# Performance work log

Hardware: AMD Instinct MI355X
Metric: run time of the kernel (lower is better)

The kernel has to match this reference:

```python
import jax, jax.numpy as jnp
import numpy as np

B, S, D, H = 2, 2048, 1024, 16
HID = 1024  # hidden_dim

def setup_inputs() -> dict:
    key = jax.random.key(0)
    ks = jax.random.split(key, 9)
    sc = 1.0 / np.sqrt(D)
    return {
        "x": jax.random.normal(ks[0], (B, S, D), dtype=jnp.float32),
        "Wq": jax.random.normal(ks[1], (HID, D), dtype=jnp.float32) * sc,
        "bq": jnp.zeros((HID,), dtype=jnp.float32),
        "Wk": jax.random.normal(ks[2], (HID, D), dtype=jnp.float32) * sc,
        "bk": jnp.zeros((HID,), dtype=jnp.float32),
        "Wv": jax.random.normal(ks[3], (HID, D), dtype=jnp.float32) * sc,
        "bv": jnp.zeros((HID,), dtype=jnp.float32),
        "Wo": jax.random.normal(ks[4], (D, HID), dtype=jnp.float32) * (1.0 / np.sqrt(HID)),
        "bo": jnp.zeros((D,), dtype=jnp.float32),
    }

def reference(x, Wq, bq, Wk, bk, Wv, bv, Wo, bo):
    num_heads = H
    hd = HID // num_heads
    q = x @ Wq.T + bq  # [B,S,HID]
    k = x @ Wk.T + bk
    v = x @ Wv.T + bv
    # [B,S,H,hd] -> [B,H,S,hd]
    q = q.reshape(B, S, num_heads, hd).transpose(0, 2, 1, 3)
    k = k.reshape(B, S, num_heads, hd).transpose(0, 2, 1, 3)
    v = v.reshape(B, S, num_heads, hd).transpose(0, 2, 1, 3)
    # NOTE: original scales by sqrt(hidden_dim), not sqrt(head_dim)
    scores = jnp.einsum('bhqd,bhkd->bhqk', q, k) / jnp.sqrt(jnp.float32(HID))
    attn = jax.nn.softmax(scores, axis=-1)
    out = jnp.einsum('bhqk,bhkd->bhqd', attn, v)  # [B,H,S,hd]
    out = out.transpose(0, 2, 1, 3).reshape(B, S, HID)
    return out @ Wo.T + bo
```

## Files before the change

### kernel.cpp

```cpp
#include <hip/hip_runtime.h>
#include <hip/hip_bf16.h>


typedef __bf16 bf16;
typedef bf16 bf16x8 __attribute__((ext_vector_type(8)));
typedef float f32x4 __attribute__((ext_vector_type(4)));

#define MFMA16(Af, Bf, Cf) __builtin_amdgcn_mfma_f32_16x16x32_bf16((Af), (Bf), (Cf), 0, 0, 0)

__device__ __forceinline__ void gl_lds16(const void* g, void* l) {
    __builtin_amdgcn_global_load_lds(
        (const __attribute__((address_space(1))) void*)g,
        (__attribute__((address_space(3))) void*)l, 16, 0, 0);
}

__device__ __forceinline__ float exp2_fast(float x) {
    float r; asm("v_exp_f32 %0, %1" : "=v"(r) : "v"(x)); return r;
}

__global__ __launch_bounds__(256) void cvt_all(
    const float* __restrict__ x, const float* __restrict__ Wq,
    const float* __restrict__ Wk, const float* __restrict__ Wv,
    const float* __restrict__ Wo,
    bf16* __restrict__ xb, bf16* __restrict__ wqb, bf16* __restrict__ wkb,
    bf16* __restrict__ wvb, bf16* __restrict__ wob)
{
    const size_t i8 = ((size_t)blockIdx.x * 256 + threadIdx.x) * 8;
    const float* src; bf16* dst; size_t off;
    if (i8 < 4194304)      { src = x;  dst = xb;  off = i8; }
    else if (i8 < 5242880) { src = Wq; dst = wqb; off = i8 - 4194304; }
    else if (i8 < 6291456) { src = Wk; dst = wkb; off = i8 - 5242880; }
    else if (i8 < 7340032) { src = Wv; dst = wvb; off = i8 - 6291456; }
    else                   { src = Wo; dst = wob; off = i8 - 7340032; }
    f32x4 a = *reinterpret_cast<const f32x4*>(src + off);
    f32x4 b = *reinterpret_cast<const f32x4*>(src + off + 4);
    bf16x8 o;
    o[0]=(bf16)a[0]; o[1]=(bf16)a[1]; o[2]=(bf16)a[2]; o[3]=(bf16)a[3];
    o[4]=(bf16)b[0]; o[5]=(bf16)b[1]; o[6]=(bf16)b[2]; o[7]=(bf16)b[3];
    *reinterpret_cast<bf16x8*>(dst + off) = o;
}

__global__ __launch_bounds__(512) void qkv_gemm(
    const bf16* __restrict__ xb,
    const bf16* __restrict__ wqb, const bf16* __restrict__ wkb,
    const bf16* __restrict__ wvb,
    const float* __restrict__ bq, const float* __restrict__ bk,
    const float* __restrict__ bv,
    bf16* __restrict__ qo, bf16* __restrict__ ko, bf16* __restrict__ vo)
{
    __shared__ bf16 As[128 * 64];
    __shared__ bf16 Bs[128 * 64];

    const int which = blockIdx.y;
    const bf16* W     = (which == 0) ? wqb : (which == 1) ? wkb : wvb;
    const float* bia  = (which == 0) ? bq : (which == 1) ? bk : bv;
    bf16* outp        = (which == 0) ? qo : (which == 1) ? ko : vo;
    const float scale = (which == 0) ? 0.04508422f : 1.0f;

    const int bid0 = blockIdx.x;
    const int xcd = bid0 & 7, j = bid0 >> 3;
    const int tm = xcd * 4 + (j & 3);
    const int tn = j >> 2;
    const int m0 = tm * 128, n0 = tn * 128;

    const int t = threadIdx.x;
    const int l = t & 63, w = t >> 6;
    const int wr = w >> 1, wc = w & 1;
    const int lg = l >> 4, lr = l & 15;

    f32x4 acc[2][4];
#pragma unroll
    for (int i = 0; i < 2; ++i)
#pragma unroll
        for (int jj = 0; jj < 4; ++jj)
            acc[i][jj] = (f32x4){0.f, 0.f, 0.f, 0.f};

    char* AsB = (char*)As;
    char* BsB = (char*)Bs;

    for (int kt = 0; kt < 1024; kt += 64) {
#pragma unroll
        for (int i = 0; i < 2; ++i) {
            const int c = w * 128 + i * 64 + l;
            const int row = c >> 3, cc = (c & 7) ^ (row & 7);
            gl_lds16(xb + (size_t)(m0 + row) * 1024 + kt + cc * 8, AsB + (w * 128 + i * 64) * 16);
            gl_lds16(W  + (size_t)(n0 + row) * 1024 + kt + cc * 8, BsB + (w * 128 + i * 64) * 16);
        }
        __syncthreads();

#pragma unroll
        for (int ks = 0; ks < 2; ++ks) {
            bf16x8 af[2], bff[4];
#pragma unroll
            for (int i = 0; i < 2; ++i) {
                const int ar = wr * 32 + i * 16 + lr;
                af[i]  = *reinterpret_cast<bf16x8*>(AsB + ar * 128 + ((ks * 64 + (lg << 4)) ^ ((ar & 7) << 4)));
            }
#pragma unroll
            for (int i = 0; i < 4; ++i) {
                const int br = wc * 64 + i * 16 + lr;
                bff[i] = *reinterpret_cast<bf16x8*>(BsB + br * 128 + ((ks * 64 + (lg << 4)) ^ ((br & 7) << 4)));
            }
            if (which == 2) {
#pragma unroll
                for (int mi = 0; mi < 2; ++mi)
#pragma unroll
                    for (int ni = 0; ni < 4; ++ni)
                        acc[mi][ni] = MFMA16(bff[ni], af[mi], acc[mi][ni]);
            } else {
#pragma unroll
                for (int mi = 0; mi < 2; ++mi)
#pragma unroll
                    for (int ni = 0; ni < 4; ++ni)
                        acc[mi][ni] = MFMA16(af[mi], bff[ni], acc[mi][ni]);
            }
        }
        __syncthreads();
    }

    if (which == 2) {
#pragma unroll
        for (int ni = 0; ni < 4; ++ni) {
#pragma unroll
            for (int mi = 0; mi < 2; ++mi) {
#pragma unroll
                for (int r = 0; r < 4; ++r) {
                    const int col = n0 + wc * 64 + ni * 16 + lg * 4 + r;
                    const int h = col >> 6, d = col & 63;
                    const int rowg = m0 + wr * 32 + mi * 16 + lr;
                    const int b = rowg >> 11, s = rowg & 2047;
                    const int key = s & 127;
                    const int pos = (key & 96) | ((key & 12) << 1) | ((key & 16) >> 2) | (key & 3);
                    const float v = acc[mi][ni][r] + bia[col];
                    outp[((size_t)(b * 16 + h) * 64 + d) * 2048 + (s & ~127) + pos] = (bf16)v;
                }
            }
        }
    } else {
#pragma unroll
        for (int ni = 0; ni < 4; ++ni) {
            const int col = n0 + wc * 64 + ni * 16 + lr;
            const float bval = bia[col];
            const int h = col >> 6, d = col & 63;
#pragma unroll
            for (int mi = 0; mi < 2; ++mi) {
#pragma unroll
                for (int r = 0; r < 4; ++r) {
                    const int rowg = m0 + wr * 32 + mi * 16 + lg * 4 + r;
                    const int b = rowg >> 11, s = rowg & 2047;
                    const float v = (acc[mi][ni][r] + bval) * scale;
                    outp[((size_t)(b * 16 + h) * 2048 + s) * 64 + d] = (bf16)v;
                }
            }
        }
    }
}

__global__ __launch_bounds__(512, 4) void attn_kernel(
    const bf16* __restrict__ qb, const bf16* __restrict__ kb,
    const bf16* __restrict__ vb, bf16* __restrict__ ao)
{
    __shared__ __align__(16) char smem[65536];

    const int bid0 = blockIdx.x;
    const int bid = ((bid0 & 7) << 6) | (bid0 >> 3);
    const int qt = bid & 15, bh = bid >> 4;
    const int b = bh >> 4, h = bh & 15;
    const bf16* qp = qb + ((size_t)bh * 2048 + qt * 128) * 64;
    const bf16* kp = kb + (size_t)bh * 2048 * 64;
    const bf16* vt = vb + (size_t)bh * 64 * 2048;

    const int t = threadIdx.x;
    const int l = t & 63, w = t >> 6;
    const int g = w >> 2, ws = w & 3;
    const int lg = l >> 4, lr = l & 15;

    bf16x8 qf[2][2];
#pragma unroll
    for (int mt = 0; mt < 2; ++mt)
#pragma unroll
        for (int ks = 0; ks < 2; ++ks)
            qf[mt][ks] = *reinterpret_cast<const bf16x8*>(
                qp + (ws * 32 + mt * 16 + lr) * 64 + ks * 32 + lg * 8);

    f32x4 oacc[2][4];
#pragma unroll
    for (int mt = 0; mt < 2; ++mt)
#pragma unroll
        for (int jj = 0; jj < 4; ++jj)
            oacc[mt][jj] = (f32x4){0.f, 0.f, 0.f, 0.f};
    f32x4 lacc[2];
    lacc[0] = (f32x4){0.f, 0.f, 0.f, 0.f};
    lacc[1] = (f32x4){0.f, 0.f, 0.f, 0.f};

    bf16x8 vone;
#pragma unroll
    for (int jj = 0; jj < 8; ++jj) vone[jj] = (bf16)1.0f;

    auto stageKV = [&](int it, char* base) {
        const int kt = g * 16 + it;
        const bf16* ksrc = kp + (size_t)kt * 4096;
        char* KsB = base + g * 8192;
        char* VtB = base + 16384 + g * 8192;
#pragma unroll
        for (int i = 0; i < 2; ++i) {
            const int c = ws * 128 + i * 64 + l;
            const int row = c >> 3, cc = (c & 7) ^ (row & 7);
            gl_lds16(ksrc + (size_t)row * 64 + cc * 8, KsB + c * 16);
        }
#pragma unroll
        for (int i = 0; i < 2; ++i) {
            const int c = ws * 128 + i * 64 + l;
            const int d = c >> 3, i16 = c & 7;
            gl_lds16(vt + (size_t)d * 2048 + kt * 64 + ((i16 ^ (d & 7)) << 3),
                     VtB + c * 16);
        }
    };

    stageKV(0, smem);
    __syncthreads();

    for (int it = 0; it < 16; ++it) {
        char* base = smem + ((it & 1) << 15);
        if (it < 15) stageKV(it + 1, smem + (((it + 1) & 1) << 15));

        char* KsB = base + g * 8192;
        char* VtB = base + 16384 + g * 8192;

        f32x4 sc[2][4];
        __builtin_amdgcn_s_setprio(1);
#pragma unroll
        for (int nt = 0; nt < 4; ++nt) {
            sc[0][nt] = (f32x4){0.f, 0.f, 0.f, 0.f};
            sc[1][nt] = (f32x4){0.f, 0.f, 0.f, 0.f};
#pragma unroll
            for (int ks = 0; ks < 2; ++ks) {
                const int nrow = nt * 16 + lr;
                bf16x8 kf = *reinterpret_cast<bf16x8*>(
                    KsB + nrow * 128 + ((ks * 64 + (lg << 4)) ^ ((nrow & 7) << 4)));
                sc[0][nt] = MFMA16(kf, qf[0][ks], sc[0][nt]);
                sc[1][nt] = MFMA16(kf, qf[1][ks], sc[1][nt]);
            }
        }
        __builtin_amdgcn_s_setprio(0);

        bf16x8 pa[2][2];
#pragma unroll
        for (int mt = 0; mt < 2; ++mt)
#pragma unroll
            for (int k4 = 0; k4 < 2; ++k4)
#pragma unroll
                for (int jj = 0; jj < 8; ++jj)
                    pa[mt][k4][jj] = (bf16)exp2_fast(sc[mt][2 * k4 + (jj >> 2)][jj & 3]);

        __builtin_amdgcn_s_setprio(1);
#pragma unroll
        for (int k4 = 0; k4 < 2; ++k4) {
            lacc[0] = MFMA16(pa[0][k4], vone, lacc[0]);
            lacc[1] = MFMA16(pa[1][k4], vone, lacc[1]);
#pragma unroll
            for (int dt = 0; dt < 4; ++dt) {
                const int d = dt * 16 + lr;
                bf16x8 vf = *reinterpret_cast<bf16x8*>(
                    VtB + d * 128 + (((k4 << 6) + (lg << 4)) ^ ((d & 7) << 4)));
                oacc[0][dt] = MFMA16(pa[0][k4], vf, oacc[0][dt]);
                oacc[1][dt] = MFMA16(pa[1][k4], vf, oacc[1][dt]);
            }
        }
        __builtin_amdgcn_s_setprio(0);

        __syncthreads();
    }

    float* cb = (float*)smem;
    const int base = (ws * 64 + l) * 21;
#pragma unroll
    for (int mt = 0; mt < 2; ++mt) {
        if (g == 1) {
#pragma unroll
            for (int dt = 0; dt < 4; ++dt)
#pragma unroll
                for (int r = 0; r < 4; ++r)
                    cb[base + dt * 4 + r] = oacc[mt][dt][r];
#pragma unroll
            for (int r = 0; r < 4; ++r)
                cb[base + 16 + r] = lacc[mt][r];
        }
        __syncthreads();
        if (g == 0) {
#pragma unroll
            for (int dt = 0; dt < 4; ++dt)
#pragma unroll
                for (int r = 0; r < 4; ++r)
                    oacc[mt][dt][r] += cb[base + dt * 4 + r];
#pragma unroll
            for (int r = 0; r < 4; ++r)
                lacc[mt][r] += cb[base + 16 + r];
        }
        __syncthreads();
    }

    if (g == 0) {
#pragma unroll
        for (int mt = 0; mt < 2; ++mt) {
            float rl[4];
#pragma unroll
            for (int r = 0; r < 4; ++r) rl[r] = 1.0f / lacc[mt][r];
#pragma unroll
            for (int dt = 0; dt < 4; ++dt) {
#pragma unroll
                for (int r = 0; r < 4; ++r) {
                    const int qrow = qt * 128 + ws * 32 + mt * 16 + lg * 4 + r;
                    const int col = h * 64 + dt * 16 + lr;
                    ao[((size_t)b * 2048 + qrow) * 1024 + col] = (bf16)(oacc[mt][dt][r] * rl[r]);
                }
            }
        }
    }
}

__global__ __launch_bounds__(512) void out_gemm(
    const bf16* __restrict__ A, const bf16* __restrict__ Wb,
    const float* __restrict__ bo, float* __restrict__ out)
{
    __shared__ bf16 As[128 * 64];
    __shared__ bf16 Bs[64 * 64];

    const int bid0 = blockIdx.x;
    const int xcd = bid0 & 7, j = bid0 >> 3;
    const int tm = xcd * 4 + (j & 3);
    const int tn = j >> 2;
    const int m0 = tm * 128, n0 = tn * 64;

    const int t = threadIdx.x;
    const int l = t & 63, w = t >> 6;
    const int wr = w >> 1, wc = w & 1;
    const int lg = l >> 4, lr = l & 15;

    f32x4 acc[2][2];
#pragma unroll
    for (int i = 0; i < 2; ++i)
#pragma unroll
        for (int jj = 0; jj < 2; ++jj)
            acc[i][jj] = (f32x4){0.f, 0.f, 0.f, 0.f};

    char* AsB = (char*)As;
    char* BsB = (char*)Bs;

    for (int kt = 0; kt < 1024; kt += 64) {
#pragma unroll
        for (int i = 0; i < 2; ++i) {
            const int c = w * 128 + i * 64 + l;
            const int row = c >> 3, cc = (c & 7) ^ (row & 7);
            gl_lds16(A + (size_t)(m0 + row) * 1024 + kt + cc * 8, AsB + (w * 128 + i * 64) * 16);
        }
        {
            const int c = w * 64 + l;
            const int row = c >> 3, cc = (c & 7) ^ (row & 7);
            gl_lds16(Wb + (size_t)(n0 + row) * 1024 + kt + cc * 8, BsB + (w * 64 + l) * 16);
        }
        __syncthreads();

#pragma unroll
        for (int ks = 0; ks < 2; ++ks) {
            bf16x8 af[2], bff[2];
#pragma unroll
            for (int i = 0; i < 2; ++i) {
                const int ar = wr * 32 + i * 16 + lr;
                af[i] = *reinterpret_cast<bf16x8*>(AsB + ar * 128 + ((ks * 64 + (lg << 4)) ^ ((ar & 7) << 4)));
            }
#pragma unroll
            for (int i = 0; i < 2; ++i) {
                const int br = wc * 32 + i * 16 + lr;
                bff[i] = *reinterpret_cast<bf16x8*>(BsB + br * 128 + ((ks * 64 + (lg << 4)) ^ ((br & 7) << 4)));
            }
#pragma unroll
            for (int mi = 0; mi < 2; ++mi)
#pragma unroll
                for (int ni = 0; ni < 2; ++ni)
                    acc[mi][ni] = MFMA16(af[mi], bff[ni], acc[mi][ni]);
        }
        __syncthreads();
    }

#pragma unroll
    for (int ni = 0; ni < 2; ++ni) {
        const int col = n0 + wc * 32 + ni * 16 + lr;
        const float bval = bo[col];
#pragma unroll
        for (int mi = 0; mi < 2; ++mi) {
#pragma unroll
            for (int r = 0; r < 4; ++r) {
                const int rowg = m0 + wr * 32 + mi * 16 + lg * 4 + r;
                out[(size_t)rowg * 1024 + col] = acc[mi][ni][r] + bval;
            }
        }
    }
}

extern "C" void kernel_launch(void* const* d_in, const int* in_sizes, int n_in,
                              void* d_out, int out_size, void* d_ws, size_t ws_size,
                              hipStream_t stream) {
    (void)in_sizes; (void)n_in; (void)out_size; (void)ws_size;
    const float* x  = (const float*)d_in[0];
    const float* Wq = (const float*)d_in[1];
    const float* bq = (const float*)d_in[2];
    const float* Wk = (const float*)d_in[3];
    const float* bk = (const float*)d_in[4];
    const float* Wv = (const float*)d_in[5];
    const float* bv = (const float*)d_in[6];
    const float* Wo = (const float*)d_in[7];
    const float* bo = (const float*)d_in[8];
    float* out = (float*)d_out;

    bf16* xb   = (bf16*)d_ws;
    bf16* wqb  = xb   + 4194304;
    bf16* wkb  = wqb  + 1048576;
    bf16* wvb  = wkb  + 1048576;
    bf16* wob  = wvb  + 1048576;
    bf16* qbuf = wob  + 1048576;
    bf16* kbuf = qbuf + 4194304;
    bf16* vbuf = kbuf + 4194304;
    bf16* aob  = vbuf + 4194304;

    cvt_all<<<4096, 256, 0, stream>>>(x, Wq, Wk, Wv, Wo, xb, wqb, wkb, wvb, wob);
    qkv_gemm<<<dim3(256, 3), 512, 0, stream>>>(xb, wqb, wkb, wvb, bq, bk, bv, qbuf, kbuf, vbuf);
    attn_kernel<<<512, 512, 0, stream>>>(qbuf, kbuf, vbuf, aob);
    out_gemm<<<512, 512, 0, stream>>>(aob, wob, bo, out);
}
```

Before: 98.25 us.

## Double-buffer LDS tiles in QKV and output GEMMs to overlap loads with MFMA

Replaces the single shared-memory A/B tiles in the QKV and output projection GEMMs with two ping-pong buffers. The load for the next k-tile is issued before the MFMA work on the current tile, so global-to-LDS transfer latency can be hidden behind compute. This doubles LDS use per block (64 KB and 48 KB), which may cut occupancy. Correctness depends on the barrier placement at the end of the loop, which is not visible here.

```diff
diff --git a/kernel.cpp b/kernel.cpp
--- a/kernel.cpp
+++ b/kernel.cpp
@@ -48,8 +48,7 @@
     const float* __restrict__ bv,
     bf16* __restrict__ qo, bf16* __restrict__ ko, bf16* __restrict__ vo)
 {
-    __shared__ bf16 As[128 * 64];
-    __shared__ bf16 Bs[128 * 64];
+    __shared__ __align__(16) char smem[65536];
 
     const int which = blockIdx.y;
     const bf16* W     = (which == 0) ? wqb : (which == 1) ? wkb : wvb;
@@ -75,18 +74,26 @@
         for (int jj = 0; jj < 4; ++jj)
             acc[i][jj] = (f32x4){0.f, 0.f, 0.f, 0.f};
 
-    char* AsB = (char*)As;
-    char* BsB = (char*)Bs;
-
-    for (int kt = 0; kt < 1024; kt += 64) {
+    auto stage = [&](int kt, char* base) {
+        char* AsB = base;
+        char* BsB = base + 16384;
 #pragma unroll
         for (int i = 0; i < 2; ++i) {
             const int c = w * 128 + i * 64 + l;
             const int row = c >> 3, cc = (c & 7) ^ (row & 7);
-            gl_lds16(xb + (size_t)(m0 + row) * 1024 + kt + cc * 8, AsB + (w * 128 + i * 64) * 16);
-            gl_lds16(W  + (size_t)(n0 + row) * 1024 + kt + cc * 8, BsB + (w * 128 + i * 64) * 16);
-        }
-        __syncthreads();
+            gl_lds16(xb + (size_t)(m0 + row) * 1024 + kt + cc * 8, AsB + c * 16);
+            gl_lds16(W  + (size_t)(n0 + row) * 1024 + kt + cc * 8, BsB + c * 16);
+        }
+    };
+
+    stage(0, smem);
+    __syncthreads();
+
+    for (int it = 0; it < 16; ++it) {
+        char* base = smem + ((it & 1) << 15);
+        if (it < 15) stage((it + 1) * 64, smem + (((it + 1) & 1) << 15));
+        char* AsB = base;
+        char* BsB = base + 16384;
 
 #pragma unroll
         for (int ks = 0; ks < 2; ++ks) {
@@ -323,8 +330,7 @@
     const bf16* __restrict__ A, const bf16* __restrict__ Wb,
     const float* __restrict__ bo, float* __restrict__ out)
 {
-    __shared__ bf16 As[128 * 64];
-    __shared__ bf16 Bs[64 * 64];
+    __shared__ __align__(16) char smem[49152];
 
     const int bid0 = blockIdx.x;
     const int xcd = bid0 & 7, j = bid0 >> 3;
@@ -344,22 +350,30 @@
         for (int jj = 0; jj < 2; ++jj)
             acc[i][jj] = (f32x4){0.f, 0.f, 0.f, 0.f};
 
-    char* AsB = (char*)As;
-    char* BsB = (char*)Bs;
-
-    for (int kt = 0; kt < 1024; kt += 64) {
+    auto stage = [&](int kt, char* base) {
+        char* AsB = base;
+        char* BsB = base + 16384;
 #pragma unroll
         for (int i = 0; i < 2; ++i) {
             const int c = w * 128 + i * 64 + l;
             const int row = c >> 3, cc = (c & 7) ^ (row & 7);
-            gl_lds16(A + (size_t)(m0 + row) * 1024 + kt + cc * 8, AsB + (w * 128 + i * 64) * 16);
+            gl_lds16(A + (size_t)(m0 + row) * 1024 + kt + cc * 8, AsB + c * 16);
         }
         {
             const int c = w * 64 + l;
             const int row = c >> 3, cc = (c & 7) ^ (row & 7);
-            gl_lds16(Wb + (size_t)(n0 + row) * 1024 + kt + cc * 8, BsB + (w * 64 + l) * 16);
-        }
-        __syncthreads();
+            gl_lds16(Wb + (size_t)(n0 + row) * 1024 + kt + cc * 8, BsB + c * 16);
+        }
+    };
+
+    stage(0, smem);
+    __syncthreads();
+
+    for (int it = 0; it < 16; ++it) {
+        char* base = smem + (it & 1) * 24576;
+        if (it < 15) stage((it + 1) * 64, smem + ((it + 1) & 1) * 24576);
+        char* AsB = base;
+        char* BsB = base + 16384;
 
 #pragma unroll
         for (int ks = 0; ks < 2; ++ks) {
```

After: 88.79 us. -9.6%, faster.
